# Performance work log

Measured on AMD Instinct MI355X. Metric: run time of the kernel, lower is better.

Reference implementation:

```python
import jax, jax.numpy as jnp
import numpy as np

D_MODEL = 1024
NUM_HEAD = 16
D_K = D_MODEL // NUM_HEAD
B, S = 2, 2048


def setup_inputs() -> dict:
    key = jax.random.key(0)
    ks = jax.random.split(key, 12)
    s = 1.0 / np.sqrt(D_MODEL)
    return {
        "x_q": jax.random.normal(ks[0], (B, S, D_MODEL), jnp.float32),
        "x_k": jax.random.normal(ks[1], (B, S, D_MODEL), jnp.float32),
        "x_v": jax.random.normal(ks[2], (B, S, D_MODEL), jnp.float32),
        "mask": jax.random.randint(ks[3], (B, S, S), 0, 2, jnp.int32),
        "Wq": jax.random.uniform(ks[4], (D_MODEL, D_MODEL), jnp.float32, -s, s),
        "bq": jax.random.uniform(ks[5], (D_MODEL,), jnp.float32, -s, s),
        "Wk": jax.random.uniform(ks[6], (D_MODEL, D_MODEL), jnp.float32, -s, s),
        "bk": jax.random.uniform(ks[7], (D_MODEL,), jnp.float32, -s, s),
        "Wv": jax.random.uniform(ks[8], (D_MODEL, D_MODEL), jnp.float32, -s, s),
        "bv": jax.random.uniform(ks[9], (D_MODEL,), jnp.float32, -s, s),
        "Wo": jax.random.uniform(ks[10], (D_MODEL, D_MODEL), jnp.float32, -s, s),
        "bo": jax.random.uniform(ks[11], (D_MODEL,), jnp.float32, -s, s),
    }


def reference(x_q, x_k, x_v, mask, Wq, bq, Wk, bk, Wv, bv, Wo, bo):
    # projections -> [B, H, S, d_k]
    def proj(x, W, b):
        y = x @ W.T + b
        return y.reshape(B, -1, NUM_HEAD, D_K).transpose(0, 2, 1, 3)

    q = proj(x_q, Wq, bq)
    k = proj(x_k, Wk, bk)
    v = proj(x_v, Wv, bv)
    scale = 1.0 / np.sqrt(D_K).astype(np.float32)
    scores = jnp.einsum("bhqd,bhkd->bhqk", q, k) * scale
    scores = jnp.where(mask[:, None, :, :] == 0, jnp.float32(-1e9), scores)
    p = jax.nn.softmax(scores, axis=-1)  # dropout is identity in eval mode
    attn = jnp.einsum("bhqk,bhkd->bhqd", p, v)
    concat = attn.transpose(0, 2, 1, 3).reshape(B, S, D_MODEL)
    return concat @ Wo.T + bo
```

## Files before the change

kernel.cpp:

```cpp
#include <hip/hip_runtime.h>
#include <cstdint>
#include <cstddef>

#define D_MODELX 1024
#define NUM_HEADX 16
#define D_KX 64
#define BBX 2
#define SSX 2048
#define M_TOK 4096
#define MBYTE (1u << 20)

typedef __attribute__((ext_vector_type(8))) short short8;
typedef __attribute__((ext_vector_type(4))) short short4v;
typedef __attribute__((ext_vector_type(4))) float float4v;
typedef __attribute__((ext_vector_type(16))) float float16v;
typedef __attribute__((ext_vector_type(2))) unsigned uint2v;
typedef __attribute__((ext_vector_type(4))) unsigned uint4v;

__device__ __forceinline__ short f2bf(float f) {
  unsigned u = __builtin_bit_cast(unsigned, f);
  u = u + 0x7FFFu + ((u >> 16) & 1u);
  return (short)(u >> 16);
}

__global__ void mask_bits_kernel(const int* __restrict__ mask, unsigned* __restrict__ mbits) {
  int i = blockIdx.x * blockDim.x + threadIdx.x;
  bool v = mask[i] != 0;
  unsigned long long bal = __ballot(v);
  int lane = threadIdx.x & 63;
  if (lane == 0)       mbits[i >> 5] = (unsigned)bal;
  else if (lane == 32) mbits[i >> 5] = (unsigned)(bal >> 32);
}

__global__ void cvt_w4_kernel(const float* __restrict__ w0, const float* __restrict__ w1,
                              const float* __restrict__ w2, const float* __restrict__ w3,
                              short* __restrict__ o0, short* __restrict__ o1,
                              short* __restrict__ o2, short* __restrict__ o3) {
  int z = blockIdx.y;
  const float* in = (z == 0) ? w0 : (z == 1) ? w1 : (z == 2) ? w2 : w3;
  short* out = (z == 0) ? o0 : (z == 1) ? o1 : (z == 2) ? o2 : o3;
  int i = blockIdx.x * blockDim.x + threadIdx.x;
  float4v v = ((const float4v*)in)[i];
  short4v s;
  s[0] = f2bf(v[0]); s[1] = f2bf(v[1]); s[2] = f2bf(v[2]); s[3] = f2bf(v[3]);
  ((short4v*)out)[i] = s;
}

__global__ void cvt_x3_kernel(const float* __restrict__ x0, const float* __restrict__ x1,
                              const float* __restrict__ x2,
                              short* __restrict__ o0, short* __restrict__ o1,
                              short* __restrict__ o2) {
  int z = blockIdx.y;
  const float* in = (z == 0) ? x0 : (z == 1) ? x1 : x2;
  short* out = (z == 0) ? o0 : (z == 1) ? o1 : o2;
  int i = blockIdx.x * blockDim.x + threadIdx.x;
  float4v v = ((const float4v*)in)[i];
  short4v s;
  s[0] = f2bf(v[0]); s[1] = f2bf(v[1]); s[2] = f2bf(v[2]); s[3] = f2bf(v[3]);
  ((short4v*)out)[i] = s;
}

#define GBK 64

__device__ __forceinline__ void gemm_body(const short* __restrict__ A,
                                          const short* __restrict__ Bw,
                                          const float* __restrict__ bias,
                                          float oscale, void* __restrict__ outp, int mode) {
  __shared__ short lds_a[128 * 64];
  __shared__ short lds_b[128 * 64];
  const int tid = threadIdx.x;
  const int lane = tid & 63;
  const int wid = tid >> 6;
  const int wm = wid >> 1, wn = wid & 1;
  const int bn = blockIdx.y >> 2;
  const int bm = (blockIdx.x << 2) | (blockIdx.y & 3);
  const int l15 = lane & 15, lg = lane >> 4;

  const int s_row = tid >> 3;
  const int s_cB = ((tid & 7) << 4) ^ ((s_row & 7) << 4);
  const short* Abase = A + (size_t)(bm * 128) * 1024 + (s_cB >> 1);
  const short* Bbase = Bw + (size_t)(bn * 128) * 1024 + (s_cB >> 1);

  const int xmask = (l15 & 7) << 4;
  const int a_b0 = (wm * 64 + l15) * 128 + ((lg * 16) ^ xmask);
  const int a_b1 = (wm * 64 + l15) * 128 + ((64 + lg * 16) ^ xmask);
  const int b_b0 = (wn * 64 + l15) * 128 + ((lg * 16) ^ xmask);
  const int b_b1 = (wn * 64 + l15) * 128 + ((64 + lg * 16) ^ xmask);

  float4v acc[4][4];
#pragma unroll
  for (int m = 0; m < 4; ++m)
#pragma unroll
    for (int n = 0; n < 4; ++n) acc[m][n] = (float4v){0.f, 0.f, 0.f, 0.f};

  for (int kt = 0; kt < 1024; kt += GBK) {
#pragma unroll
    for (int it = 0; it < 4; ++it) {
      int row = it * 32 + s_row;
      __builtin_amdgcn_global_load_lds(
          (const uint32_t*)(Abase + (size_t)row * 1024 + kt),
          (uint32_t*)(lds_a + (it * 256 + wid * 64) * 8), 16, 0, 0);
      __builtin_amdgcn_global_load_lds(
          (const uint32_t*)(Bbase + (size_t)row * 1024 + kt),
          (uint32_t*)(lds_b + (it * 256 + wid * 64) * 8), 16, 0, 0);
    }
    __syncthreads();

    short8 af[4][2];
#pragma unroll
    for (int m = 0; m < 4; ++m) {
      af[m][0] = *(const short8*)((const char*)lds_a + a_b0 + m * 2048);
      af[m][1] = *(const short8*)((const char*)lds_a + a_b1 + m * 2048);
    }
#pragma unroll
    for (int n = 0; n < 4; ++n) {
      short8 b0 = *(const short8*)((const char*)lds_b + b_b0 + n * 2048);
      short8 b1 = *(const short8*)((const char*)lds_b + b_b1 + n * 2048);
#pragma unroll
      for (int m = 0; m < 4; ++m) {
        acc[m][n] = __builtin_amdgcn_mfma_f32_16x16x32_bf16(af[m][0], b0, acc[m][n], 0, 0, 0);
        acc[m][n] = __builtin_amdgcn_mfma_f32_16x16x32_bf16(af[m][1], b1, acc[m][n], 0, 0, 0);
      }
    }
    __syncthreads();
  }

#pragma unroll
  for (int n = 0; n < 4; ++n) {
    int col = bn * 128 + wn * 64 + n * 16 + l15;
    float bv = bias[col];
#pragma unroll
    for (int m = 0; m < 4; ++m) {
      if (mode == 2) {
        int base_row = bm * 128 + wm * 64 + m * 16 + lg * 4;
        int bidx = base_row >> 11, s = base_row & 2047;
        int h = col >> 6, d = col & 63;
        short4v sv;
#pragma unroll
        for (int r = 0; r < 4; ++r) sv[r] = f2bf(acc[m][n][r] + bv);
        *(short4v*)&((short*)outp)[(((size_t)(bidx * NUM_HEADX + h)) * D_KX + d) * SSX + s] = sv;
      } else {
#pragma unroll
        for (int r = 0; r < 4; ++r) {
          int row = bm * 128 + wm * 64 + m * 16 + lg * 4 + r;
          float val = (acc[m][n][r] + bv) * oscale;
          if (mode == 0) {
            int bidx = row >> 11, s = row & 2047;
            int h = col >> 6, d = col & 63;
            ((short*)outp)[(((size_t)(bidx * NUM_HEADX + h)) * SSX + s) * D_KX + d] = f2bf(val);
          } else {
            ((float*)outp)[(size_t)row * D_MODELX + col] = val;
          }
        }
      }
    }
  }
}

__global__ __launch_bounds__(256) void gemm_qkv_kernel(
    const short* __restrict__ xq, const short* __restrict__ xk, const short* __restrict__ xv,
    const short* __restrict__ wq, const short* __restrict__ wk, const short* __restrict__ wv,
    const float* __restrict__ bq, const float* __restrict__ bk, const float* __restrict__ bv,
    short* __restrict__ qo, short* __restrict__ ko, short* __restrict__ vo, float qs) {
  int z = blockIdx.z;
  const short* A = (z == 0) ? xq : (z == 1) ? xk : xv;
  const short* W = (z == 0) ? wq : (z == 1) ? wk : wv;
  const float* bi = (z == 0) ? bq : (z == 1) ? bk : bv;
  void* out = (z == 0) ? (void*)qo : (z == 1) ? (void*)ko : (void*)vo;
  float os = (z == 0) ? qs : 1.0f;
  int mode = (z == 2) ? 2 : 0;
  gemm_body(A, W, bi, os, out, mode);
}

__global__ __launch_bounds__(256) void gemm_one_kernel(const short* __restrict__ A,
                                                       const short* __restrict__ W,
                                                       const float* __restrict__ bias,
                                                       float os, void* __restrict__ out, int mode) {
  gemm_body(A, W, bias, os, out, mode);
}

__global__ __launch_bounds__(256, 2) void attn_kernel(const short* __restrict__ q_ws,
                                                      const short* __restrict__ k_ws,
                                                      const short* __restrict__ vT_ws,
                                                      const unsigned* __restrict__ mbits,
                                                      short* __restrict__ attn_ws,
                                                      short* __restrict__ opart,
                                                      float* __restrict__ lpart) {
  __shared__ short k_lds[2][4096];
  __shared__ short vT_lds[2][4096];

  const int tid = threadIdx.x;
  const int lane = tid & 63;
  const int w = tid >> 6;
  const int l31 = lane & 31, hi = lane >> 5;
  const int bid0 = blockIdx.x;
  const int bid = ((bid0 & 7) << 6) | (bid0 >> 3);
  const int qt = bid & 15;
  const int bh = bid >> 4;
  const int b = bh >> 4;
  const int h = bh & 15;
  const int z = blockIdx.z;
  const int nsplit = gridDim.z;
  const int nt = (SSX / 64) / nsplit;
  const int kb0 = z * nt * 64;

  const int qrow = qt * 128 + w * 32;
  const int q = qrow + l31;

  const int xm = (lane & 7) << 4;
  int rd[4];
#pragma unroll
  for (int j = 0; j < 4; ++j) rd[j] = l31 * 128 + ((j * 32 + hi * 16) ^ xm);
  char* kbase = (char*)k_lds;
  char* vbase = (char*)vT_lds;

  const int srow = tid >> 2;
  const int scolS = (tid & 3) * 16;
  const int st0 = srow * 128 + ((scolS * 2) ^ ((srow & 7) << 4));
  const int st1 = srow * 128 + ((scolS * 2 + 16) ^ ((srow & 7) << 4));

  const short* kp = k_ws + (size_t)bh * SSX * D_KX + (size_t)srow * D_KX + scolS;
  const short* vp = vT_ws + (size_t)bh * D_KX * SSX + (size_t)srow * SSX + scolS;

  short8 qf[4];
#pragma unroll
  for (int ds = 0; ds < 4; ++ds)
    qf[ds] = *(const short8*)(q_ws + ((size_t)bh * SSX + q) * D_KX + ds * 16 + hi * 8);

  float16v acc[2];
#pragma unroll
  for (int db = 0; db < 2; ++db)
#pragma unroll
    for (int i = 0; i < 16; ++i) acc[db][i] = 0.f;
  float l_own = 0.f;

  short8 kr0, kr1, vr0, vr1;
  auto loadt = [&](int kb) {
    const short* kq = kp + (size_t)kb * D_KX;
    kr0 = *(const short8*)kq;
    kr1 = *(const short8*)(kq + 8);
    const short* vq = vp + kb;
    vr0 = *(const short8*)vq;
    vr1 = *(const short8*)(vq + 8);
  };
  auto storet = [&](int BUF) {
    *(short8*)(kbase + BUF + st0) = kr0;
    *(short8*)(kbase + BUF + st1) = kr1;
    *(short8*)(vbase + BUF + st0) = vr0;
    *(short8*)(vbase + BUF + st1) = vr1;
  };

  const unsigned* mrow = mbits + ((size_t)b * SSX + q) * (SSX / 32) + (kb0 >> 5);
  unsigned long long mw = *(const unsigned long long*)mrow, mwn = 0;

  loadt(kb0);
  storet(0);
  loadt(kb0 + 64);
  __syncthreads();

  auto step = [&](int t, int CURB, int NXTB) {
    unsigned long long shv = mw >> (hi * 4);

    auto do_kb = [&](const float16v& s, int kb, int CURB_) {
      unsigned wvm = (kb == 0) ? (unsigned)shv : (unsigned)(shv >> 32);
      unsigned cw[8];
      float ls = 0.f;
#pragma unroll
      for (int qd = 0; qd < 4; ++qd) {
        float pv_[4];
#pragma unroll
        for (int r = 0; r < 4; ++r) {
          float e = __builtin_amdgcn_exp2f(s[qd * 4 + r]);
          e = ((wvm >> (qd * 8 + r)) & 1u) ? e : 0.f;
          ls += e;
          pv_[r] = e;
        }
        unsigned u0, u1;
        asm("v_cvt_pk_bf16_f32 %0, %1, %2" : "=v"(u0) : "v"(pv_[0]), "v"(pv_[1]));
        asm("v_cvt_pk_bf16_f32 %0, %1, %2" : "=v"(u1) : "v"(pv_[2]), "v"(pv_[3]));
        cw[qd * 2] = u0;
        cw[qd * 2 + 1] = u1;
      }
      l_own += ls;
#pragma unroll
      for (int g = 0; g < 2; ++g) {
        unsigned a0 = cw[2 * g * 2],     b0 = cw[(2 * g + 1) * 2];
        unsigned a1 = cw[2 * g * 2 + 1], b1 = cw[(2 * g + 1) * 2 + 1];
        asm("v_permlane32_swap_b32 %0, %1" : "+v"(a0), "+v"(b0));
        asm("v_permlane32_swap_b32 %0, %1" : "+v"(a1), "+v"(b1));
        short8 Bf = __builtin_bit_cast(short8, (uint4v){a0, a1, b0, b1});
        __builtin_amdgcn_s_setprio(1);
#pragma unroll
        for (int db = 0; db < 2; ++db) {
          short8 vf = *(const short8*)(vbase + CURB_ + db * 4096 + rd[kb * 2 + g]);
          acc[db] = __builtin_amdgcn_mfma_f32_32x32x16_bf16(vf, Bf, acc[db], 0, 0, 0);
        }
        __builtin_amdgcn_s_setprio(0);
      }
    };

    float16v s0, s1;
#pragma unroll
    for (int i = 0; i < 16; ++i) { s0[i] = 0.f; s1[i] = 0.f; }
    __builtin_amdgcn_s_setprio(1);
#pragma unroll
    for (int ds = 0; ds < 4; ++ds) {
      short8 ka = *(const short8*)(kbase + CURB + rd[ds]);
      short8 kb_ = *(const short8*)(kbase + CURB + 4096 + rd[ds]);
      s0 = __builtin_amdgcn_mfma_f32_32x32x16_bf16(ka, qf[ds], s0, 0, 0, 0);
      s1 = __builtin_amdgcn_mfma_f32_32x32x16_bf16(kb_, qf[ds], s1, 0, 0, 0);
    }
    __builtin_amdgcn_s_setprio(0);

    if (t < nt - 1) storet(NXTB);
    if (t < nt - 2) loadt(kb0 + (t + 2) * 64);
    if (t < nt - 1) mwn = *(const unsigned long long*)(mrow + 2 * (t + 1));

    do_kb(s0, 0, CURB);
    do_kb(s1, 1, CURB);

    __syncthreads();
    mw = mwn;
  };

  for (int t2 = 0; t2 < nt / 2; ++t2) {
    step(2 * t2, 0, 8192);
    step(2 * t2 + 1, 8192, 0);
  }

  float lp = l_own + __shfl_xor(l_own, 32);
  if (nsplit == 1) {
    float inv = 1.0f / lp;
    size_t ttok = (size_t)b * SSX + q;
#pragma unroll
    for (int db = 0; db < 2; ++db)
#pragma unroll
      for (int qd = 0; qd < 4; ++qd) {
        short4v sv;
#pragma unroll
        for (int r = 0; r < 4; ++r) sv[r] = f2bf(acc[db][qd * 4 + r] * inv);
        *(short4v*)&attn_ws[ttok * D_MODELX + h * 64 + db * 32 + qd * 8 + hi * 4] = sv;
      }
  } else {
    size_t rowp = ((size_t)z * 32 + bh) * SSX + q;
    if (hi == 0) lpart[rowp] = lp;
#pragma unroll
    for (int db = 0; db < 2; ++db)
#pragma unroll
      for (int qd = 0; qd < 4; ++qd) {
        short4v sv;
#pragma unroll
        for (int r = 0; r < 4; ++r) sv[r] = f2bf(acc[db][qd * 4 + r]);
        *(short4v*)&opart[rowp * D_KX + db * 32 + qd * 8 + hi * 4] = sv;
      }
  }
}

__global__ void combine_kernel(const short* __restrict__ opart, const float* __restrict__ lpart,
                               short* __restrict__ attn_ws) {
  int gtid = blockIdx.x * blockDim.x + threadIdx.x;
  int row = gtid >> 3;
  int dc = (gtid & 7) * 8;
  int bh = row >> 11, s = row & 2047;
  int b = bh >> 4, h = bh & 15;
  float inv = 1.0f / (lpart[row] + lpart[row + 32 * SSX]);
  short8 o0 = *(const short8*)&opart[(size_t)row * D_KX + dc];
  short8 o1 = *(const short8*)&opart[((size_t)row + 32 * SSX) * D_KX + dc];
  short8 sv;
#pragma unroll
  for (int j = 0; j < 8; ++j) {
    float f0 = __builtin_bit_cast(float, ((unsigned)(unsigned short)o0[j]) << 16);
    float f1 = __builtin_bit_cast(float, ((unsigned)(unsigned short)o1[j]) << 16);
    sv[j] = f2bf((f0 + f1) * inv);
  }
  *(short8*)&attn_ws[(((size_t)b * SSX + s) * D_MODELX) + h * 64 + dc] = sv;
}

extern "C" void kernel_launch(void* const* d_in, const int* in_sizes, int n_in,
                              void* d_out, int out_size, void* d_ws, size_t ws_size,
                              hipStream_t stream) {
  const float* x_q = (const float*)d_in[0];
  const float* x_k = (const float*)d_in[1];
  const float* x_v = (const float*)d_in[2];
  const int*   mask = (const int*)d_in[3];
  const float* Wq = (const float*)d_in[4];
  const float* bq = (const float*)d_in[5];
  const float* Wk = (const float*)d_in[6];
  const float* bk = (const float*)d_in[7];
  const float* Wv = (const float*)d_in[8];
  const float* bv = (const float*)d_in[9];
  const float* Wo = (const float*)d_in[10];
  const float* bo = (const float*)d_in[11];

  const float QSCALE = 0.125f * 1.44269504089f;

  char* ws = (char*)d_ws;
  short* q_ws  = (short*)(ws + 0 * MBYTE);
  short* k_ws  = (short*)(ws + 8 * MBYTE);
  short* vT_ws = (short*)(ws + 16 * MBYTE);

  dim3 ggrid(D_MODELX / 128, M_TOK / 128);

  if (ws_size >= (size_t)56 * MBYTE) {
    short* wq_bf = (short*)(ws + 24 * MBYTE);
    short* wk_bf = (short*)(ws + 26 * MBYTE);
    short* wv_bf = (short*)(ws + 28 * MBYTE);
    short* wo_bf = (short*)(ws + 30 * MBYTE);
    short* xq_bf = (short*)(ws + 32 * MBYTE);
    short* xk_bf = (short*)(ws + 40 * MBYTE);
    short* xv_bf = (short*)(ws + 48 * MBYTE);
    unsigned* mbits = (unsigned*)(ws + 24 * MBYTE);
    float* lpart    = (float*)(ws + 25 * MBYTE);
    short* attn_ws  = (short*)(ws + 32 * MBYTE);
    short* opart    = (short*)(ws + 40 * MBYTE);

    cvt_w4_kernel<<<dim3(1024, 4), 256, 0, stream>>>(Wq, Wk, Wv, Wo, wq_bf, wk_bf, wv_bf, wo_bf);
    cvt_x3_kernel<<<dim3(4096, 3), 256, 0, stream>>>(x_q, x_k, x_v, xq_bf, xk_bf, xv_bf);

    dim3 qkvgrid(D_MODELX / 128, M_TOK / 128, 3);
    gemm_qkv_kernel<<<qkvgrid, 256, 0, stream>>>(xq_bf, xk_bf, xv_bf, wq_bf, wk_bf, wv_bf,
                                                 bq, bk, bv, q_ws, k_ws, vT_ws, QSCALE);

    mask_bits_kernel<<<(BBX * SSX * SSX) / 256, 256, 0, stream>>>(mask, mbits);

    dim3 agrid(BBX * NUM_HEADX * (SSX / 128), 1, 2);
    attn_kernel<<<agrid, 256, 0, stream>>>(q_ws, k_ws, vT_ws, mbits, attn_ws, opart, lpart);
    combine_kernel<<<2048, 256, 0, stream>>>(opart, lpart, attn_ws);

    gemm_one_kernel<<<ggrid, 256, 0, stream>>>(attn_ws, wo_bf, bo, 1.0f, d_out, 1);
  } else {
    unsigned* mbits = (unsigned*)(ws + 24 * MBYTE);
    short* w_bf = (short*)(ws + 25 * MBYTE);
    short* x_bf = (short*)(ws + 27 * MBYTE);
    short* attn_ws = (short*)(ws + 27 * MBYTE);

    mask_bits_kernel<<<(BBX * SSX * SSX) / 256, 256, 0, stream>>>(mask, mbits);

    cvt_w4_kernel<<<dim3(1024, 1), 256, 0, stream>>>(Wq, Wq, Wq, Wq, w_bf, w_bf, w_bf, w_bf);
    cvt_x3_kernel<<<dim3(4096, 1), 256, 0, stream>>>(x_q, x_q, x_q, x_bf, x_bf, x_bf);
    gemm_one_kernel<<<ggrid, 256, 0, stream>>>(x_bf, w_bf, bq, QSCALE, q_ws, 0);

    cvt_w4_kernel<<<dim3(1024, 1), 256, 0, stream>>>(Wk, Wk, Wk, Wk, w_bf, w_bf, w_bf, w_bf);
    cvt_x3_kernel<<<dim3(4096, 1), 256, 0, stream>>>(x_k, x_k, x_k, x_bf, x_bf, x_bf);
    gemm_one_kernel<<<ggrid, 256, 0, stream>>>(x_bf, w_bf, bk, 1.0f, k_ws, 0);

    cvt_w4_kernel<<<dim3(1024, 1), 256, 0, stream>>>(Wv, Wv, Wv, Wv, w_bf, w_bf, w_bf, w_bf);
    cvt_x3_kernel<<<dim3(4096, 1), 256, 0, stream>>>(x_v, x_v, x_v, x_bf, x_bf, x_bf);
    gemm_one_kernel<<<ggrid, 256, 0, stream>>>(x_bf, w_bf, bv, 1.0f, vT_ws, 2);

    dim3 agrid(BBX * NUM_HEADX * (SSX / 128), 1, 1);
    attn_kernel<<<agrid, 256, 0, stream>>>(q_ws, k_ws, vT_ws, mbits, attn_ws, nullptr, nullptr);

    cvt_w4_kernel<<<dim3(1024, 1), 256, 0, stream>>>(Wo, Wo, Wo, Wo, w_bf, w_bf, w_bf, w_bf);
    gemm_one_kernel<<<ggrid, 256, 0, stream>>>(attn_ws, w_bf, bo, 1.0f, d_out, 1);
  }
}
```

Before: 158.0 us.

## Stage K/V tiles via direct global-to-LDS loads with pre-swizzled layouts

The attention kernel now copies K and V^T tiles straight from global memory into LDS with global_load_lds, in place of loading into registers and storing to LDS. This removes the register round trip and the VGPR pressure of holding a prefetched tile. Because direct loads cannot apply the per-thread XOR swizzle, the QKV projection GEMM now writes K and V^T already swizzled (new mode 3 for K, an XOR on the s index for V). The prefetch depth drops from register-staged two-ahead to a single next-tile LDS stage issued at the start of each step.

```diff
diff --git a/kernel.cpp b/kernel.cpp
--- a/kernel.cpp
+++ b/kernel.cpp
@@ -138,16 +138,18 @@
         short4v sv;
 #pragma unroll
         for (int r = 0; r < 4; ++r) sv[r] = f2bf(acc[m][n][r] + bv);
-        *(short4v*)&((short*)outp)[(((size_t)(bidx * NUM_HEADX + h)) * D_KX + d) * SSX + s] = sv;
+        int sw = s ^ ((d & 7) << 3);
+        *(short4v*)&((short*)outp)[(((size_t)(bidx * NUM_HEADX + h)) * D_KX + d) * SSX + sw] = sv;
       } else {
 #pragma unroll
         for (int r = 0; r < 4; ++r) {
           int row = bm * 128 + wm * 64 + m * 16 + lg * 4 + r;
           float val = (acc[m][n][r] + bv) * oscale;
-          if (mode == 0) {
+          if (mode == 0 || mode == 3) {
             int bidx = row >> 11, s = row & 2047;
             int h = col >> 6, d = col & 63;
-            ((short*)outp)[(((size_t)(bidx * NUM_HEADX + h)) * SSX + s) * D_KX + d] = f2bf(val);
+            int dd = (mode == 3) ? (d ^ ((s & 7) << 3)) : d;
+            ((short*)outp)[(((size_t)(bidx * NUM_HEADX + h)) * SSX + s) * D_KX + dd] = f2bf(val);
           } else {
             ((float*)outp)[(size_t)row * D_MODELX + col] = val;
           }
@@ -168,7 +170,7 @@
   const float* bi = (z == 0) ? bq : (z == 1) ? bk : bv;
   void* out = (z == 0) ? (void*)qo : (z == 1) ? (void*)ko : (void*)vo;
   float os = (z == 0) ? qs : 1.0f;
-  int mode = (z == 2) ? 2 : 0;
+  int mode = (z == 2) ? 2 : (z == 1) ? 3 : 0;
   gemm_body(A, W, bi, os, out, mode);
 }
 
@@ -214,13 +216,20 @@
   char* kbase = (char*)k_lds;
   char* vbase = (char*)vT_lds;
 
-  const int srow = tid >> 2;
-  const int scolS = (tid & 3) * 16;
-  const int st0 = srow * 128 + ((scolS * 2) ^ ((srow & 7) << 4));
-  const int st1 = srow * 128 + ((scolS * 2 + 16) ^ ((srow & 7) << 4));
-
-  const short* kp = k_ws + (size_t)bh * SSX * D_KX + (size_t)srow * D_KX + scolS;
-  const short* vp = vT_ws + (size_t)bh * D_KX * SSX + (size_t)srow * SSX + scolS;
+  const short* ksrc = k_ws + (size_t)bh * SSX * D_KX;
+  const short* vsrc0 = vT_ws + (size_t)bh * D_KX * SSX + (size_t)(tid >> 3) * SSX + (tid & 7) * 8;
+  const short* vsrc1 = vsrc0 + (size_t)32 * SSX;
+
+  auto stage = [&](int kb, int BUF) {
+    __builtin_amdgcn_global_load_lds((const uint32_t*)(ksrc + (size_t)kb * 64 + tid * 8),
+        (uint32_t*)(kbase + BUF + tid * 16), 16, 0, 0);
+    __builtin_amdgcn_global_load_lds((const uint32_t*)(ksrc + (size_t)kb * 64 + 2048 + tid * 8),
+        (uint32_t*)(kbase + BUF + 4096 + tid * 16), 16, 0, 0);
+    __builtin_amdgcn_global_load_lds((const uint32_t*)(vsrc0 + kb),
+        (uint32_t*)(vbase + BUF + tid * 16), 16, 0, 0);
+    __builtin_amdgcn_global_load_lds((const uint32_t*)(vsrc1 + kb),
+        (uint32_t*)(vbase + BUF + 4096 + tid * 16), 16, 0, 0);
+  };
 
   short8 qf[4];
 #pragma unroll
@@ -234,31 +243,18 @@
     for (int i = 0; i < 16; ++i) acc[db][i] = 0.f;
   float l_own = 0.f;
 
-  short8 kr0, kr1, vr0, vr1;
-  auto loadt = [&](int kb) {
-    const short* kq = kp + (size_t)kb * D_KX;
-    kr0 = *(const short8*)kq;
-    kr1 = *(const short8*)(kq + 8);
-    const short* vq = vp + kb;
-    vr0 = *(const short8*)vq;
-    vr1 = *(const short8*)(vq + 8);
-  };
-  auto storet = [&](int BUF) {
-    *(short8*)(kbase + BUF + st0) = kr0;
-    *(short8*)(kbase + BUF + st1) = kr1;
-    *(short8*)(vbase + BUF + st0) = vr0;
-    *(short8*)(vbase + BUF + st1) = vr1;
-  };
-
   const unsigned* mrow = mbits + ((size_t)b * SSX + q) * (SSX / 32) + (kb0 >> 5);
   unsigned long long mw = *(const unsigned long long*)mrow, mwn = 0;
 
-  loadt(kb0);
-  storet(0);
-  loadt(kb0 + 64);
+  stage(kb0, 0);
   __syncthreads();
 
   auto step = [&](int t, int CURB, int NXTB) {
+    if (t < nt - 1) {
+      stage(kb0 + (t + 1) * 64, NXTB);
+      mwn = *(const unsigned long long*)(mrow + 2 * (t + 1));
+    }
+
     unsigned long long shv = mw >> (hi * 4);
 
     auto do_kb = [&](const float16v& s, int kb, int CURB_) {
@@ -311,10 +307,6 @@
       s1 = __builtin_amdgcn_mfma_f32_32x32x16_bf16(kb_, qf[ds], s1, 0, 0, 0);
     }
     __builtin_amdgcn_s_setprio(0);
-
-    if (t < nt - 1) storet(NXTB);
-    if (t < nt - 2) loadt(kb0 + (t + 2) * 64);
-    if (t < nt - 1) mwn = *(const unsigned long long*)(mrow + 2 * (t + 1));
 
     do_kb(s0, 0, CURB);
     do_kb(s1, 1, CURB);
@@ -442,7 +434,7 @@
 
     cvt_w4_kernel<<<dim3(1024, 1), 256, 0, stream>>>(Wk, Wk, Wk, Wk, w_bf, w_bf, w_bf, w_bf);
     cvt_x3_kernel<<<dim3(4096, 1), 256, 0, stream>>>(x_k, x_k, x_k, x_bf, x_bf, x_bf);
-    gemm_one_kernel<<<ggrid, 256, 0, stream>>>(x_bf, w_bf, bk, 1.0f, k_ws, 0);
+    gemm_one_kernel<<<ggrid, 256, 0, stream>>>(x_bf, w_bf, bk, 1.0f, k_ws, 3);
 
     cvt_w4_kernel<<<dim3(1024, 1), 256, 0, stream>>>(Wv, Wv, Wv, Wv, w_bf, w_bf, w_bf, w_bf);
     cvt_x3_kernel<<<dim3(4096, 1), 256, 0, stream>>>(x_v, x_v, x_v, x_bf, x_bf, x_bf);
```

Result: slower. 163.7 us (+3.6%).
